# Kernel optimization log

Measured on AMD Instinct MI355X. Metric: run time of the kernel, lower is better.

The kernel has to match this reference:

```python
import jax, jax.numpy as jnp
import numpy as np

NEG_INF = -1e12
ALPHA = 0.01  # LeakyReLU slope


def setup_inputs() -> dict:
    key = jax.random.key(0)
    ks = jax.random.split(key, 12)
    K, N, DIN, H1, DOUT, FC1 = 64, 1024, 16, 4, 8, 54
    X = jax.random.normal(ks[0], (K, N, DIN), dtype=jnp.float32)
    adj = jax.random.randint(ks[1], (N, N), 0, 2, dtype=jnp.int32)
    # Xavier-uniform-ish init scale (gain 1.414)
    def xavier(k, shape):
        fan_in, fan_out = shape[0], shape[-1]
        lim = 1.414 * np.sqrt(6.0 / (fan_in + fan_out))
        return jax.random.uniform(k, shape, jnp.float32, -lim, lim)
    W1 = xavier(ks[2], (DIN, H1))
    a1 = xavier(ks[3], (2 * H1, 1))
    W2 = xavier(ks[4], (H1, DOUT))
    a2 = xavier(ks[5], (2 * DOUT, 1))
    fc1_w = xavier(ks[6], (N * DOUT, FC1))
    fc1_b = jnp.zeros((FC1,), jnp.float32)
    out_w = xavier(ks[7], (FC1, N))
    out_b = jnp.zeros((N,), jnp.float32)
    return {"X": X, "adj": adj, "W1": W1, "a1": a1, "W2": W2, "a2": a2,
            "fc1_w": fc1_w, "fc1_b": fc1_b, "out_w": out_w, "out_b": out_b}


def _gat_layer(h_in, adj, W, a):
    # h: [K, N, F]
    h = jnp.matmul(h_in, W)
    Fdim = W.shape[1]
    # concat(h_i, h_j) @ a  ==  (h_i . a[:F]) + (h_j . a[F:])
    f1 = jnp.matmul(h, a[:Fdim, 0])  # [K, N]
    f2 = jnp.matmul(h, a[Fdim:, 0])  # [K, N]
    e = jax.nn.leaky_relu(f1[:, :, None] + f2[:, None, :], ALPHA)  # [K, N, N]
    e = jnp.where(adj[None, :, :] > 0, e, NEG_INF)
    att = jax.nn.softmax(e, axis=2)
    return jnp.einsum('kij,kjf->kif', att, h)


def reference(X, adj, W1, a1, W2, a2, fc1_w, fc1_b, out_w, out_b):
    x = jax.nn.relu(_gat_layer(X, adj, W1, a1))
    x = jax.nn.relu(_gat_layer(x, adj, W2, a2))
    x = x.reshape(x.shape[0], -1)  # [K, N*dim_output]
    x = jax.nn.relu(jnp.matmul(x, fc1_w) + fc1_b)
    return jnp.matmul(x, out_w) + out_b  # [K, N] q-values
```

## Files before the change

### kernel.cpp

```cpp
#include <hip/hip_runtime.h>
#include <hip/hip_bf16.h>

constexpr int K    = 64;
constexpr int N    = 1024;
constexpr int DIN  = 16;
constexpr int H1   = 4;
constexpr int DOUT = 8;
constexpr int FC1  = 54;

#define ALPHA_F   (0.01f)
#define LOG2E_F   (1.4426950408889634f)

typedef unsigned int uint;
typedef short  bf16x8 __attribute__((ext_vector_type(8)));
typedef float  f32x4  __attribute__((ext_vector_type(4)));

__device__ inline float fast_exp2(float x) {
#if __has_builtin(__builtin_amdgcn_exp2f)
    return __builtin_amdgcn_exp2f(x);
#else
    return __expf(x * 0.6931471805599453f);
#endif
}

__device__ inline uint pk_bf16(float a, float b) {
    union { __hip_bfloat162 h; uint u; } v;
    v.h = __float22bfloat162_rn(make_float2(a, b));
    return v.u;
}


__global__ __launch_bounds__(512) void prep_kernel(
        const int* __restrict__ adj, unsigned long long* __restrict__ maskM,
        const float* __restrict__ fc1w, float* __restrict__ wt,
        const float* __restrict__ X, const float* __restrict__ W1,
        const float* __restrict__ a1,
        uint4* __restrict__ HB1, float* __restrict__ f11, float* __restrict__ f21) {
    int b = blockIdx.x;
    if (b < 2048) {
        int wave = threadIdx.x >> 6, lane = threadIdx.x & 63;
        int wid = b * 8 + wave;
        int jw  = wid >> 10;
        int i   = wid & 1023;
        int v = adj[i * N + (jw << 6) + lane];
        unsigned long long m = __ballot(v > 0);
        if (lane == 0) maskM[i * 16 + jw] = m;
    } else if (b < 2112) {
        __shared__ float tile[128 * FC1];
        const int m0 = (b - 2048) * 128;
        const float* src = fc1w + (size_t)m0 * FC1;
        for (int idx = threadIdx.x; idx < 128 * FC1; idx += 512)
            tile[idx] = src[idx];
        __syncthreads();
        for (int idx = threadIdx.x; idx < 128 * FC1; idx += 512) {
            int c = idx >> 7, mm = idx & 127;
            wt[(size_t)c * (N * DOUT) + m0 + mm] = tile[mm * FC1 + c];
        }
    } else {
        __shared__ float hrow[512 * 4];
        const int bb  = b - 2112;
        const int k   = bb >> 1;
        const int j0  = (bb & 1) * 512;
        const int tid = threadIdx.x;
        const int idx = k * N + j0 + tid;
        const float4* x4 = (const float4*)(X + (size_t)idx * DIN);
        float hv_[H1] = {0.f, 0.f, 0.f, 0.f};
        #pragma unroll
        for (int q = 0; q < 4; q++) {
            float4 xv = x4[q];
            #pragma unroll
            for (int f = 0; f < H1; f++) {
                hv_[f] += xv.x * W1[(q * 4 + 0) * H1 + f] + xv.y * W1[(q * 4 + 1) * H1 + f]
                        + xv.z * W1[(q * 4 + 2) * H1 + f] + xv.w * W1[(q * 4 + 3) * H1 + f];
            }
        }
        float s1 = 0.f, s2 = 0.f;
        #pragma unroll
        for (int f = 0; f < H1; f++) { s1 += hv_[f] * a1[f]; s2 += hv_[f] * a1[H1 + f]; }
        f11[idx] = s1 * LOG2E_F;
        f21[idx] = s2 * LOG2E_F;
        #pragma unroll
        for (int f = 0; f < H1; f++) hrow[tid * 4 + f] = hv_[f];
        __syncthreads();
        uint4* HBk = HB1 + (size_t)k * 2048 + (j0 >> 5) * 64;
        #pragma unroll
        for (int e = tid; e < 1024; e += 512) {
            int cl = e >> 6, l = e & 63, q = (l >> 4), n = l & 15;
            uint4 dw;
            if (n < H1) {
                const float* hp = hrow + (cl * 32 + q * 8) * 4 + n;
                dw.x = pk_bf16(hp[0],  hp[4]);
                dw.y = pk_bf16(hp[8],  hp[12]);
                dw.z = pk_bf16(hp[16], hp[20]);
                dw.w = pk_bf16(hp[24], hp[28]);
            } else if (n == H1) {
                dw = make_uint4(0x3f803f80u, 0x3f803f80u, 0x3f803f80u, 0x3f803f80u);
            } else {
                dw = make_uint4(0u, 0u, 0u, 0u);
            }
            HBk[cl * 64 + l] = dw;
        }
    }
}

template <int F, bool FUSE>
__global__ __launch_bounds__(512, 4) void gat_attn_mfma(
        const unsigned long long* __restrict__ maskM,
        const uint4* __restrict__ HBin,
        const float* __restrict__ f1,
        const float* __restrict__ f2,
        const float* __restrict__ W2,
        const float* __restrict__ a2,
        uint4* __restrict__ HBout,
        float* __restrict__ o_x,
        float* __restrict__ o_f1,
        float* __restrict__ o_f2) {
    __shared__ float F2s[1024];
    __shared__ float XPa[8][16][5];
    __shared__ float XPb[8][16][9];

    const int tid  = threadIdx.x;
    const int lane = tid & 63;
    const int wv   = tid >> 6;
    const int quad = lane >> 4;
    const int n16  = lane & 15;
    const int k    = blockIdx.x >> 3;

    if (tid < 256)
        ((float4*)F2s)[tid] = ((const float4*)(f2 + k * N))[tid];
    __syncthreads();

    const int itile = (blockIdx.x & 7) * 8 + wv;
    const int ibase = itile * 16;
    const int irow  = ibase + n16;
    const float f1v = f1[k * N + irow];
    const uint4* mrow = (const uint4*)((const char*)maskM + (size_t)irow * 128);
    const uint4* HBk  = HBin + (size_t)k * 2048;

    f32x4 acc = {0.f, 0.f, 0.f, 0.f};
    union { bf16x8 v; uint u[4]; } af;
    union { bf16x8 v; uint4 q; }  bfrag;

    #pragma unroll 2
    for (int g = 0; g < 8; g++) {
        const uint4 Mg = mrow[g];
        #pragma unroll
        for (int cc = 0; cc < 4; cc++) {
            const int c = g * 4 + cc;
            const uint mdw = (cc == 0) ? Mg.x : (cc == 1) ? Mg.y
                           : (cc == 2) ? Mg.z : Mg.w;
            const uint mb  = (mdw >> (quad * 8)) & 0xffu;
            float4 fa = *(const float4*)(F2s + c * 32 + quad * 8);
            float4 fb = *(const float4*)(F2s + c * 32 + quad * 8 + 4);
            bfrag.q = HBk[c * 64 + lane];
            float f2e[8] = {fa.x, fa.y, fa.z, fa.w, fb.x, fb.y, fb.z, fb.w};
            float pv[8];
            #pragma unroll
            for (int jj = 0; jj < 8; jj++) {
                float x = f1v + f2e[jj];
                float e = fmaxf(x, ALPHA_F * x);
                float p = fast_exp2(e);
                pv[jj] = (mb & (1u << jj)) ? p : 0.f;
            }
            #pragma unroll
            for (int pr = 0; pr < 4; pr++)
                af.u[pr] = pk_bf16(pv[2 * pr], pv[2 * pr + 1]);
            acc = __builtin_amdgcn_mfma_f32_16x16x32_bf16(af.v, bfrag.v, acc, 0, 0, 0);
        }
    }

    #pragma unroll
    for (int r = 0; r < 4; r++) {
        float den = __shfl(acc[r], (lane & 48) + F);
        float inv = (den > 0.f) ? 1.f / den : 0.f;
        float xo  = fmaxf(acc[r] * inv, 0.f);
        int m = quad * 4 + r;
        if constexpr (FUSE) {
            if (n16 < F) XPa[wv][m][n16] = xo;
        } else {
            if (n16 < F) o_x[((size_t)k * N + ibase + m) * F + n16] = xo;
        }
    }

    if constexpr (FUSE) {
        __syncthreads();
        if (lane < 16) {
            const int m = lane;
            float x0 = XPa[wv][m][0], x1 = XPa[wv][m][1];
            float x2v = XPa[wv][m][2], x3 = XPa[wv][m][3];
            float hv[DOUT];
            #pragma unroll
            for (int f = 0; f < DOUT; f++) {
                hv[f] = x0 * W2[f]      + x1 * W2[8 + f]
                      + x2v * W2[16 + f] + x3 * W2[24 + f];
            }
            float t1 = 0.f, t2 = 0.f;
            #pragma unroll
            for (int f = 0; f < DOUT; f++) { t1 += hv[f] * a2[f]; t2 += hv[f] * a2[DOUT + f]; }
            const int row = k * N + ibase + m;
            o_f1[row] = t1 * LOG2E_F;
            o_f2[row] = t2 * LOG2E_F;
            #pragma unroll
            for (int f = 0; f < DOUT; f++) XPb[wv][m][f] = hv[f];
        }
        __syncthreads();
        if (lane < 32) {
            const int c2    = ibase >> 5;
            const int qhalf = (ibase >> 4) & 1;
            const int ql    = lane >> 4;
            const int n     = lane & 15;
            const int q     = qhalf * 2 + ql;
            uint4 dw;
            if (n < DOUT) {
                dw.x = pk_bf16(XPb[wv][ql * 8 + 0][n], XPb[wv][ql * 8 + 1][n]);
                dw.y = pk_bf16(XPb[wv][ql * 8 + 2][n], XPb[wv][ql * 8 + 3][n]);
                dw.z = pk_bf16(XPb[wv][ql * 8 + 4][n], XPb[wv][ql * 8 + 5][n]);
                dw.w = pk_bf16(XPb[wv][ql * 8 + 6][n], XPb[wv][ql * 8 + 7][n]);
            } else if (n == DOUT) {
                dw = make_uint4(0x3f803f80u, 0x3f803f80u, 0x3f803f80u, 0x3f803f80u);
            } else {
                dw = make_uint4(0u, 0u, 0u, 0u);
            }
            HBout[(size_t)k * 2048 + c2 * 64 + q * 16 + n] = dw;
        }
    }
}

__global__ __launch_bounds__(256) void fc1_kernel(
        const float* __restrict__ x2, const float* __restrict__ wt,
        const float* __restrict__ b, float* __restrict__ y) {
    const int bid  = blockIdx.x;
    const int k    = bid / FC1;
    const int c    = bid - k * FC1;
    const int wave = threadIdx.x >> 6;
    const int lane = threadIdx.x & 63;
    const float4* x4 = (const float4*)(x2 + (size_t)k * N * DOUT) + wave * 512 + lane;
    const float4* w4 = (const float4*)(wt + (size_t)c * N * DOUT) + wave * 512 + lane;
    float s0 = 0.f, s1 = 0.f;
    #pragma unroll
    for (int q = 0; q < 8; q += 2) {
        float4 a0 = x4[q * 64],      w0 = w4[q * 64];
        float4 a1 = x4[q * 64 + 64], w1 = w4[q * 64 + 64];
        s0 += a0.x * w0.x + a0.y * w0.y + a0.z * w0.z + a0.w * w0.w;
        s1 += a1.x * w1.x + a1.y * w1.y + a1.z * w1.z + a1.w * w1.w;
    }
    float s = s0 + s1;
    #pragma unroll
    for (int off = 32; off > 0; off >>= 1) s += __shfl_xor(s, off);
    __shared__ float red[4];
    if (lane == 0) red[wave] = s;
    __syncthreads();
    if (threadIdx.x == 0)
        y[bid] = fmaxf(red[0] + red[1] + red[2] + red[3] + b[c], 0.f);
}

__global__ void fc2_kernel(const float* __restrict__ y,
                           const float* __restrict__ out_w,
                           const float* __restrict__ out_b,
                           float* __restrict__ out) {
    int n = blockIdx.x * blockDim.x + threadIdx.x;
    int k = blockIdx.y;
    const float* yk = y + (size_t)k * FC1;
    float s = out_b[n];
    #pragma unroll 6
    for (int c = 0; c < FC1; c++) s += yk[c] * out_w[(size_t)c * N + n];
    out[(size_t)k * N + n] = s;
}

extern "C" void kernel_launch(void* const* d_in, const int* in_sizes, int n_in,
                              void* d_out, int out_size, void* d_ws, size_t ws_size,
                              hipStream_t stream) {
    const float* X     = (const float*)d_in[0];
    const int*   adj   = (const int*)  d_in[1];
    const float* W1    = (const float*)d_in[2];
    const float* a1    = (const float*)d_in[3];
    const float* W2    = (const float*)d_in[4];
    const float* a2    = (const float*)d_in[5];
    const float* fc1w  = (const float*)d_in[6];
    const float* fc1b  = (const float*)d_in[7];
    const float* outw  = (const float*)d_in[8];
    const float* outb  = (const float*)d_in[9];
    float* out = (float*)d_out;

    float* ws  = (float*)d_ws;
    float* f11 = ws;
    float* f21 = f11 + 65536;
    float* f12 = f21 + 65536;
    float* f22 = f12 + 65536;
    float* x2  = f22 + 65536;
    float* y   = x2  + 524288;
    float* wt  = y   + 4096;
    unsigned long long* mM = (unsigned long long*)(wt + 442368);
    uint4* HB1 = (uint4*)(wt + 442368 + 32768);
    uint4* HB2 = HB1 + 131072;

    prep_kernel<<<dim3(2240), dim3(512), 0, stream>>>(
        adj, mM, fc1w, wt, X, W1, a1, HB1, f11, f21);

    gat_attn_mfma<4, true><<<dim3(K * 8), dim3(512), 0, stream>>>(
        mM, HB1, f11, f21, W2, a2, HB2, nullptr, f12, f22);

    gat_attn_mfma<8, false><<<dim3(K * 8), dim3(512), 0, stream>>>(
        mM, HB2, f12, f22, nullptr, nullptr, nullptr, x2, nullptr, nullptr);

    fc1_kernel<<<dim3(K * FC1), dim3(256), 0, stream>>>(x2, wt, fc1b, y);
    fc2_kernel<<<dim3(N / 256, K), dim3(256), 0, stream>>>(y, outw, outb, out);
}
```

Baseline: 134.7 us.

## Split attention key range across wave halves and double grid size

Each block now covers 4 row tiles instead of 8. Its two wave groups each handle half of the 1024 key columns (split-K), and the partial MFMA accumulators are combined through shared memory before normalisation. The grid doubles to K*16 blocks and launch bounds ask for higher occupancy. This shortens each wave's serial loop and raises parallelism, at the cost of an extra barrier and reduction, reloading F2s per block, and idle waves during the epilogue.

```diff
diff --git a/kernel.cpp b/kernel.cpp
--- a/kernel.cpp
+++ b/kernel.cpp
@@ -104,7 +104,7 @@
 }
 
 template <int F, bool FUSE>
-__global__ __launch_bounds__(512, 4) void gat_attn_mfma(
+__global__ __launch_bounds__(512, 8) void gat_attn_mfma(
         const unsigned long long* __restrict__ maskM,
         const uint4* __restrict__ HBin,
         const float* __restrict__ f1,
@@ -116,43 +116,47 @@
         float* __restrict__ o_f1,
         float* __restrict__ o_f2) {
     __shared__ float F2s[1024];
-    __shared__ float XPa[8][16][5];
-    __shared__ float XPb[8][16][9];
+    __shared__ float CMB[4][4][64];
+    __shared__ float XPa[4][16][5];
+    __shared__ float XPb[4][16][9];
 
     const int tid  = threadIdx.x;
     const int lane = tid & 63;
     const int wv   = tid >> 6;
+    const int wt4  = wv & 3;
+    const int jh   = wv >> 2;
     const int quad = lane >> 4;
     const int n16  = lane & 15;
-    const int k    = blockIdx.x >> 3;
+    const int k    = blockIdx.x >> 4;
 
     if (tid < 256)
         ((float4*)F2s)[tid] = ((const float4*)(f2 + k * N))[tid];
     __syncthreads();
 
-    const int itile = (blockIdx.x & 7) * 8 + wv;
+    const int itile = (blockIdx.x & 15) * 4 + wt4;
     const int ibase = itile * 16;
     const int irow  = ibase + n16;
     const float f1v = f1[k * N + irow];
-    const uint4* mrow = (const uint4*)((const char*)maskM + (size_t)irow * 128);
-    const uint4* HBk  = HBin + (size_t)k * 2048;
+    const uint4* mrow = (const uint4*)((const char*)maskM + (size_t)irow * 128) + jh * 4;
+    const uint4* HBk  = HBin + (size_t)k * 2048 + jh * 1024;
 
     f32x4 acc = {0.f, 0.f, 0.f, 0.f};
     union { bf16x8 v; uint u[4]; } af;
     union { bf16x8 v; uint4 q; }  bfrag;
 
     #pragma unroll 2
-    for (int g = 0; g < 8; g++) {
+    for (int g = 0; g < 4; g++) {
         const uint4 Mg = mrow[g];
         #pragma unroll
         for (int cc = 0; cc < 4; cc++) {
-            const int c = g * 4 + cc;
+            const int cl = g * 4 + cc;
+            const int c  = jh * 16 + cl;
             const uint mdw = (cc == 0) ? Mg.x : (cc == 1) ? Mg.y
                            : (cc == 2) ? Mg.z : Mg.w;
             const uint mb  = (mdw >> (quad * 8)) & 0xffu;
+            bfrag.q = HBk[cl * 64 + lane];
             float4 fa = *(const float4*)(F2s + c * 32 + quad * 8);
             float4 fb = *(const float4*)(F2s + c * 32 + quad * 8 + 4);
-            bfrag.q = HBk[c * 64 + lane];
             float f2e[8] = {fa.x, fa.y, fa.z, fa.w, fb.x, fb.y, fb.z, fb.w};
             float pv[8];
             #pragma unroll
@@ -169,25 +173,35 @@
         }
     }
 
-    #pragma unroll
-    for (int r = 0; r < 4; r++) {
-        float den = __shfl(acc[r], (lane & 48) + F);
-        float inv = (den > 0.f) ? 1.f / den : 0.f;
-        float xo  = fmaxf(acc[r] * inv, 0.f);
-        int m = quad * 4 + r;
-        if constexpr (FUSE) {
-            if (n16 < F) XPa[wv][m][n16] = xo;
-        } else {
-            if (n16 < F) o_x[((size_t)k * N + ibase + m) * F + n16] = xo;
+    if (jh == 1) {
+        #pragma unroll
+        for (int r = 0; r < 4; r++) CMB[wt4][r][lane] = acc[r];
+    }
+    __syncthreads();
+
+    if (jh == 0) {
+        #pragma unroll
+        for (int r = 0; r < 4; r++) acc[r] += CMB[wt4][r][lane];
+        #pragma unroll
+        for (int r = 0; r < 4; r++) {
+            float den = __shfl(acc[r], (lane & 48) + F);
+            float inv = (den > 0.f) ? 1.f / den : 0.f;
+            float xo  = fmaxf(acc[r] * inv, 0.f);
+            int m = quad * 4 + r;
+            if constexpr (FUSE) {
+                if (n16 < F) XPa[wt4][m][n16] = xo;
+            } else {
+                if (n16 < F) o_x[((size_t)k * N + ibase + m) * F + n16] = xo;
+            }
         }
     }
 
     if constexpr (FUSE) {
         __syncthreads();
-        if (lane < 16) {
+        if (jh == 0 && lane < 16) {
             const int m = lane;
-            float x0 = XPa[wv][m][0], x1 = XPa[wv][m][1];
-            float x2v = XPa[wv][m][2], x3 = XPa[wv][m][3];
+            float x0 = XPa[wt4][m][0], x1 = XPa[wt4][m][1];
+            float x2v = XPa[wt4][m][2], x3 = XPa[wt4][m][3];
             float hv[DOUT];
             #pragma unroll
             for (int f = 0; f < DOUT; f++) {
@@ -201,10 +215,10 @@
             o_f1[row] = t1 * LOG2E_F;
             o_f2[row] = t2 * LOG2E_F;
             #pragma unroll
-            for (int f = 0; f < DOUT; f++) XPb[wv][m][f] = hv[f];
+            for (int f = 0; f < DOUT; f++) XPb[wt4][m][f] = hv[f];
         }
         __syncthreads();
-        if (lane < 32) {
+        if (jh == 0 && lane < 32) {
             const int c2    = ibase >> 5;
             const int qhalf = (ibase >> 4) & 1;
             const int ql    = lane >> 4;
@@ -212,10 +226,10 @@
             const int q     = qhalf * 2 + ql;
             uint4 dw;
             if (n < DOUT) {
-                dw.x = pk_bf16(XPb[wv][ql * 8 + 0][n], XPb[wv][ql * 8 + 1][n]);
-                dw.y = pk_bf16(XPb[wv][ql * 8 + 2][n], XPb[wv][ql * 8 + 3][n]);
-                dw.z = pk_bf16(XPb[wv][ql * 8 + 4][n], XPb[wv][ql * 8 + 5][n]);
-                dw.w = pk_bf16(XPb[wv][ql * 8 + 6][n], XPb[wv][ql * 8 + 7][n]);
+                dw.x = pk_bf16(XPb[wt4][ql * 8 + 0][n], XPb[wt4][ql * 8 + 1][n]);
+                dw.y = pk_bf16(XPb[wt4][ql * 8 + 2][n], XPb[wt4][ql * 8 + 3][n]);
+                dw.z = pk_bf16(XPb[wt4][ql * 8 + 4][n], XPb[wt4][ql * 8 + 5][n]);
+                dw.w = pk_bf16(XPb[wt4][ql * 8 + 6][n], XPb[wt4][ql * 8 + 7][n]);
             } else if (n == DOUT) {
                 dw = make_uint4(0x3f803f80u, 0x3f803f80u, 0x3f803f80u, 0x3f803f80u);
             } else {
@@ -297,10 +311,10 @@
     prep_kernel<<<dim3(2240), dim3(512), 0, stream>>>(
         adj, mM, fc1w, wt, X, W1, a1, HB1, f11, f21);
 
-    gat_attn_mfma<4, true><<<dim3(K * 8), dim3(512), 0, stream>>>(
+    gat_attn_mfma<4, true><<<dim3(K * 16), dim3(512), 0, stream>>>(
         mM, HB1, f11, f21, W2, a2, HB2, nullptr, f12, f22);
 
-    gat_attn_mfma<8, false><<<dim3(K * 8), dim3(512), 0, stream>>>(
+    gat_attn_mfma<8, false><<<dim3(K * 16), dim3(512), 0, stream>>>(
         mM, HB2, f12, f22, nullptr, nullptr, nullptr, x2, nullptr, nullptr);
 
     fc1_kernel<<<dim3(K * FC1), dim3(256), 0, stream>>>(x2, wt, fc1b, y);
```

Result: no change. 134.8 us (+0.1%).
